# Optimization experiments

Hardware: AMD Instinct MI355X
Metric: run time of the kernel (lower is better)

The kernel has to match this reference:

```python
import jax, jax.numpy as jnp
import numpy as np
import math

D_MODEL = 1024
NUM_HEADS = 16
D_K = D_MODEL // NUM_HEADS
B, S = 2, 2048


def setup_inputs() -> dict:
    key = jax.random.key(0)
    ks = jax.random.split(key, 11)
    scale = 1.0 / math.sqrt(D_MODEL)
    inp = {
        "query": jax.random.normal(ks[0], (B, S, D_MODEL), jnp.float32),
        "key": jax.random.normal(ks[1], (B, S, D_MODEL), jnp.float32),
        "value": jax.random.normal(ks[2], (B, S, D_MODEL), jnp.float32),
        "Wq": jax.random.normal(ks[3], (D_MODEL, D_MODEL), jnp.float32) * scale,
        "bq": jnp.zeros((D_MODEL,), jnp.float32),
        "Wk": jax.random.normal(ks[4], (D_MODEL, D_MODEL), jnp.float32) * scale,
        "bk": jnp.zeros((D_MODEL,), jnp.float32),
        "Wv": jax.random.normal(ks[5], (D_MODEL, D_MODEL), jnp.float32) * scale,
        "bv": jnp.zeros((D_MODEL,), jnp.float32),
        "Wo": jax.random.normal(ks[6], (D_MODEL, D_MODEL), jnp.float32) * scale,
        "bo": jnp.zeros((D_MODEL,), jnp.float32),
    }
    return inp


def reference(query, key, value, Wq, bq, Wk, bk, Wv, bv, Wo, bo):
    b, s, _ = query.shape
    # QKV projections (torch Linear: x @ W.T + b)
    Q = query @ Wq.T + bq
    K = key @ Wk.T + bk
    V = value @ Wv.T + bv
    # [b, h, s, d_k]
    Q = Q.reshape(b, s, NUM_HEADS, D_K).transpose(0, 2, 1, 3)
    K = K.reshape(b, s, NUM_HEADS, D_K).transpose(0, 2, 1, 3)
    V = V.reshape(b, s, NUM_HEADS, D_K).transpose(0, 2, 1, 3)
    score = jnp.einsum("bhqd,bhkd->bhqk", Q, K) / math.sqrt(D_K)
    attn = jax.nn.softmax(score, axis=-1)
    out = jnp.einsum("bhqk,bhkd->bhqd", attn, V)
    out = out.transpose(0, 2, 1, 3).reshape(b, s, D_MODEL)
    return out @ Wo.T + bo
```

## Files before the change

### kernel.cpp

```cpp
#include <hip/hip_runtime.h>

#define NHEADS 16
#define SEQ    2048
#define BATCH  2
#define DMODEL 1024
#define MTOT   4096

typedef __attribute__((ext_vector_type(8)))  short short8;
typedef __attribute__((ext_vector_type(4)))  float f32x4;
typedef __attribute__((ext_vector_type(16))) float f32x16;

__device__ __forceinline__ unsigned short f32_to_bf16_rn(float x) {
  unsigned int u = __float_as_uint(x);
  u += 0x7fffu + ((u >> 16) & 1u);
  return (unsigned short)(u >> 16);
}

__device__ __forceinline__ unsigned cvt_pk_bf16(float lo, float hi_) {
  unsigned r;
  asm("v_cvt_pk_bf16_f32 %0, %1, %2" : "=v"(r) : "v"(lo), "v"(hi_));
  return r;
}

__device__ __forceinline__ void permlane32_swap(unsigned &a, unsigned &b) {
  asm("v_permlane32_swap_b32 %0, %1" : "+v"(a), "+v"(b));
}

__device__ __forceinline__ void async16(void* lds, const void* g) {
  __builtin_amdgcn_global_load_lds((const __attribute__((address_space(1))) unsigned int*)g,
                                   (__attribute__((address_space(3))) unsigned int*)lds, 16, 0, 0);
}

__global__ void cvt_bf16_kernel(const float* __restrict__ x0, const float* __restrict__ x1,
                                const float* __restrict__ x2,
                                const float* __restrict__ w0, const float* __restrict__ w1,
                                const float* __restrict__ w2, const float* __restrict__ w3,
                                unsigned short* __restrict__ obase)
{
  const int e = (blockIdx.x*256 + threadIdx.x)*8;
  const float* src;
  int local;
  if (e < 3*4194304) {
    const int t = e >> 22;
    src = t==0 ? x0 : t==1 ? x1 : x2;
    local = e & (4194304-1);
    src += local;
    local += t << 22;
  } else {
    const int f = e - 3*4194304;
    const int t = f >> 20;
    src = t==0 ? w0 : t==1 ? w1 : t==2 ? w2 : w3;
    src += (f & (1048576-1));
    local = e;
  }
  const float4 v0 = *(const float4*)(src);
  const float4 v1 = *(const float4*)(src + 4);
  union { unsigned short u[8]; uint4 v; } r;
  r.u[0] = f32_to_bf16_rn(v0.x); r.u[1] = f32_to_bf16_rn(v0.y);
  r.u[2] = f32_to_bf16_rn(v0.z); r.u[3] = f32_to_bf16_rn(v0.w);
  r.u[4] = f32_to_bf16_rn(v1.x); r.u[5] = f32_to_bf16_rn(v1.y);
  r.u[6] = f32_to_bf16_rn(v1.z); r.u[7] = f32_to_bf16_rn(v1.w);
  *(uint4*)(obase + local) = r.v;
}

template<int BM>
__device__ __forceinline__ void gemm_core(const unsigned short* __restrict__ A,
                                          const unsigned short* __restrict__ W,
                                          unsigned short* sA, unsigned short* sB,
                                          int m0, int n0, f32x4 (&acc)[BM/32][4])
{
  constexpr int MI = BM/32;
  const int t = threadIdx.x;
  const int lane = t & 63;
  const int wv = t >> 6;
  const int wm = wv >> 1, wn = wv & 1;
  const int lr = lane & 15, lk = lane >> 4;

  for (int kt = 0; kt < DMODEL/64; ++kt) {
    #pragma unroll
    for (int g = 0; g < MI; ++g) {
      const int o  = g*4096 + t*16;
      const int so = o ^ (((o >> 7) & 7) << 4);
      const int row = so >> 7, colE = (so & 127) >> 1;
      async16((char*)sA + o, A + (size_t)(m0 + row)*DMODEL + kt*64 + colE);
    }
    #pragma unroll
    for (int g = 0; g < 4; ++g) {
      const int o  = g*4096 + t*16;
      const int so = o ^ (((o >> 7) & 7) << 4);
      const int row = so >> 7, colE = (so & 127) >> 1;
      async16((char*)sB + o, W + (size_t)(n0 + row)*DMODEL + kt*64 + colE);
    }
    __syncthreads();
    #pragma unroll
    for (int ks = 0; ks < 2; ++ks) {
      short8 af[MI], bf[4];
      #pragma unroll
      for (int mi = 0; mi < MI; ++mi) {
        const int row = wm*(BM/2) + mi*16 + lr;
        const int sl  = (ks*4 + lk) ^ (row & 7);
        af[mi] = *(const short8*)(sA + row*64 + sl*8);
      }
      #pragma unroll
      for (int ni = 0; ni < 4; ++ni) {
        const int row = wn*64 + ni*16 + lr;
        const int sl  = (ks*4 + lk) ^ (row & 7);
        bf[ni] = *(const short8*)(sB + row*64 + sl*8);
      }
      #pragma unroll
      for (int mi = 0; mi < MI; ++mi)
        #pragma unroll
        for (int ni = 0; ni < 4; ++ni)
          acc[mi][ni] = __builtin_amdgcn_mfma_f32_16x16x32_bf16(af[mi], bf[ni], acc[mi][ni], 0, 0, 0);
    }
    __syncthreads();
  }
}

__global__ __launch_bounds__(256, 2)
void qkv_gemm_kernel(const unsigned short* __restrict__ Xq, const unsigned short* __restrict__ Xk,
                     const unsigned short* __restrict__ Xv,
                     const unsigned short* __restrict__ Wq, const unsigned short* __restrict__ Wk,
                     const unsigned short* __restrict__ Wv,
                     const float* __restrict__ bq, const float* __restrict__ bk,
                     const float* __restrict__ bv,
                     unsigned short* __restrict__ Qp, unsigned short* __restrict__ Kp,
                     unsigned short* __restrict__ Vtp)
{
  constexpr int BM = 128;
  constexpr int MI = BM/32;
  __shared__ __align__(16) unsigned short sA[BM*64];
  __shared__ __align__(16) unsigned short sB[128*64];

  const int m0   = blockIdx.x * BM;
  const int nabs = blockIdx.y * 128;
  const int wsel = nabs >> 10;
  const int n0   = nabs & 1023;
  const unsigned short* A = wsel==0 ? Xq : wsel==1 ? Xk : Xv;
  const unsigned short* W = wsel==0 ? Wq : wsel==1 ? Wk : Wv;
  const float* bias       = wsel==0 ? bq : wsel==1 ? bk : bv;
  unsigned short* dst     = wsel==0 ? Qp : wsel==1 ? Kp : Vtp;

  f32x4 acc[MI][4];
  #pragma unroll
  for (int mi = 0; mi < MI; ++mi)
    #pragma unroll
    for (int ni = 0; ni < 4; ++ni)
      acc[mi][ni] = {0.f, 0.f, 0.f, 0.f};

  gemm_core<BM>(A, W, sA, sB, m0, n0, acc);

  const int t = threadIdx.x, lane = t & 63, wvx = t >> 6;
  const int wm = wvx >> 1, wn = wvx & 1;
  const int lr = lane & 15, lk = lane >> 4;
  const float qscale = (wsel == 0) ? 0.125f * 1.4426950408889634f : 1.0f;

  #pragma unroll
  for (int ni = 0; ni < 4; ++ni) {
    const int nn = n0 + wn*64 + ni*16 + lr;
    const float badd = bias[nn];
    const int hh = nn >> 6, d = nn & 63;
    #pragma unroll
    for (int mi = 0; mi < MI; ++mi) {
      #pragma unroll
      for (int r = 0; r < 4; ++r) {
        const int m = m0 + wm*(BM/2) + mi*16 + lk*4 + r;
        const int bb = m >> 11, s = m & 2047;
        const float v = (acc[mi][ni][r] + badd) * qscale;
        size_t idx;
        if (wsel == 2) idx = (((size_t)bb*NHEADS + hh)*64 + d)*SEQ + s;
        else           idx = (((size_t)bb*NHEADS + hh)*SEQ + s)*64 + d;
        dst[idx] = f32_to_bf16_rn(v);
      }
    }
  }
}

__global__ __launch_bounds__(256, 2)
void attn_kernel(const unsigned short* __restrict__ Qp, const unsigned short* __restrict__ Kp,
                 const unsigned short* __restrict__ Vtp, unsigned short* __restrict__ Op)
{
  __shared__ __align__(16) unsigned short sm[16384];

  const int t = threadIdx.x, lane = t & 63, w = t >> 6;
  const int lq = lane & 31, hi = lane >> 5;
  const int qt = blockIdx.x, h = blockIdx.y, b = blockIdx.z;
  const size_t bh = (size_t)b*NHEADS + h;
  const unsigned short* Qh = Qp  + bh*SEQ*64;
  const unsigned short* Kh = Kp  + bh*SEQ*64;
  const unsigned short* Vh = Vtp + bh*64*SEQ;
  const int q0 = qt*128 + w*32;

  short8 qf[4];
  #pragma unroll
  for (int ks = 0; ks < 4; ++ks)
    qf[ks] = *(const short8*)(Qh + (size_t)(q0 + lq)*64 + ks*16 + hi*8);

  union { unsigned u[4]; short8 s; } ones;
  #pragma unroll
  for (int i = 0; i < 4; ++i) ones.u[i] = 0x3F803F80u;

  const unsigned short* srcp;
  size_t sstride;
  if (w < 2) { srcp = Kh + (size_t)(w*32 + lq)*64 + hi*8;        sstride = 64*64; }
  else       { srcp = Vh + (size_t)((w-2)*32 + lq)*2048 + hi*8;  sstride = 64;    }

  #pragma unroll
  for (int i = 0; i < 4; ++i)
    async16((char*)sm + w*4096 + i*1024, srcp + i*16);
  srcp += sstride;
  asm volatile("s_waitcnt vmcnt(0)" ::: "memory");
  __syncthreads();

  f32x16 o[2], ls;
  #pragma unroll
  for (int d = 0; d < 2; ++d)
    #pragma unroll
    for (int r = 0; r < 16; ++r) o[d][r] = 0.f;
  #pragma unroll
  for (int r = 0; r < 16; ++r) ls[r] = 0.f;

  #pragma unroll 2
  for (int kt = 0; kt < SEQ/64; ++kt) {
    if (kt + 1 < SEQ/64) {
      const int nb = ((kt + 1) & 1) * 16384;
      #pragma unroll
      for (int i = 0; i < 4; ++i)
        async16((char*)sm + nb + w*4096 + i*1024, srcp + i*16);
      srcp += sstride;
    }
    const unsigned short* base  = sm + (kt & 1)*8192;
    const unsigned short* vbase = base + 4096;

    f32x16 st[2];
    #pragma unroll
    for (int s = 0; s < 2; ++s)
      #pragma unroll
      for (int r = 0; r < 16; ++r) st[s][r] = 0.f;
    __builtin_amdgcn_s_setprio(1);
    #pragma unroll
    for (int sub = 0; sub < 2; ++sub)
      #pragma unroll
      for (int ks = 0; ks < 4; ++ks) {
        const short8 kf = *(const short8*)(base + (sub*4 + ks)*512 + lane*8);
        st[sub] = __builtin_amdgcn_mfma_f32_32x32x16_bf16(kf, qf[ks], st[sub], 0, 0, 0);
      }
    __builtin_amdgcn_s_setprio(0);

    #pragma unroll
    for (int s = 0; s < 2; ++s)
      #pragma unroll
      for (int r = 0; r < 16; ++r)
        st[s][r] = __builtin_amdgcn_exp2f(st[s][r]);

    #pragma unroll
    for (int sub = 0; sub < 2; ++sub) {
      union { unsigned u[4]; short8 s; } pA, pB;
      {
        unsigned x0 = cvt_pk_bf16(st[sub][0],  st[sub][1]);
        unsigned x1 = cvt_pk_bf16(st[sub][2],  st[sub][3]);
        unsigned y0 = cvt_pk_bf16(st[sub][4],  st[sub][5]);
        unsigned y1 = cvt_pk_bf16(st[sub][6],  st[sub][7]);
        permlane32_swap(x0, y0);
        permlane32_swap(x1, y1);
        pA.u[0] = x0; pA.u[1] = x1; pA.u[2] = y0; pA.u[3] = y1;
        unsigned z0 = cvt_pk_bf16(st[sub][8],  st[sub][9]);
        unsigned z1 = cvt_pk_bf16(st[sub][10], st[sub][11]);
        unsigned w0 = cvt_pk_bf16(st[sub][12], st[sub][13]);
        unsigned w1 = cvt_pk_bf16(st[sub][14], st[sub][15]);
        permlane32_swap(z0, w0);
        permlane32_swap(z1, w1);
        pB.u[0] = z0; pB.u[1] = z1; pB.u[2] = w0; pB.u[3] = w1;
      }
      const short8 v00 = *(const short8*)(vbase + (0*4 + 2*sub    )*512 + lane*8);
      const short8 v01 = *(const short8*)(vbase + (0*4 + 2*sub + 1)*512 + lane*8);
      const short8 v10 = *(const short8*)(vbase + (1*4 + 2*sub    )*512 + lane*8);
      const short8 v11 = *(const short8*)(vbase + (1*4 + 2*sub + 1)*512 + lane*8);
      __builtin_amdgcn_s_setprio(1);
      o[0] = __builtin_amdgcn_mfma_f32_32x32x16_bf16(v00, pA.s, o[0], 0, 0, 0);
      o[1] = __builtin_amdgcn_mfma_f32_32x32x16_bf16(v10, pA.s, o[1], 0, 0, 0);
      ls   = __builtin_amdgcn_mfma_f32_32x32x16_bf16(ones.s, pA.s, ls, 0, 0, 0);
      o[0] = __builtin_amdgcn_mfma_f32_32x32x16_bf16(v01, pB.s, o[0], 0, 0, 0);
      o[1] = __builtin_amdgcn_mfma_f32_32x32x16_bf16(v11, pB.s, o[1], 0, 0, 0);
      ls   = __builtin_amdgcn_mfma_f32_32x32x16_bf16(ones.s, pB.s, ls, 0, 0, 0);
      __builtin_amdgcn_s_setprio(0);
    }
    asm volatile("s_waitcnt vmcnt(0)" ::: "memory");
    __syncthreads();
  }

  const float inv = __builtin_amdgcn_rcpf(ls[0]);
  unsigned short* orow = Op + ((size_t)b*SEQ + q0 + lq)*DMODEL + h*64;
  #pragma unroll
  for (int dblk = 0; dblk < 2; ++dblk)
    #pragma unroll
    for (int g = 0; g < 4; ++g) {
      union { unsigned short us[4]; uint2 v; } pk;
      #pragma unroll
      for (int r = 0; r < 4; ++r) pk.us[r] = f32_to_bf16_rn(o[dblk][g*4 + r] * inv);
      *(uint2*)(orow + dblk*32 + g*8 + hi*4) = pk.v;
    }
}

__global__ __launch_bounds__(256, 2)
void oproj_gemm_kernel(const unsigned short* __restrict__ Oin, const unsigned short* __restrict__ Wo,
                       const float* __restrict__ bo, float* __restrict__ out)
{
  constexpr int BM = 64;
  constexpr int MI = BM/32;
  __shared__ __align__(16) unsigned short sA[BM*64];
  __shared__ __align__(16) unsigned short sB[128*64];
  const int m0 = blockIdx.x * BM;
  const int n0 = blockIdx.y * 128;

  f32x4 acc[MI][4];
  #pragma unroll
  for (int mi = 0; mi < MI; ++mi)
    #pragma unroll
    for (int ni = 0; ni < 4; ++ni)
      acc[mi][ni] = {0.f,0.f,0.f,0.f};

  gemm_core<BM>(Oin, Wo, sA, sB, m0, n0, acc);

  const int t = threadIdx.x, lane = t & 63, wvx = t >> 6;
  const int wm = wvx >> 1, wn = wvx & 1;
  const int lr = lane & 15, lk = lane >> 4;

  #pragma unroll
  for (int ni = 0; ni < 4; ++ni) {
    const int nn = n0 + wn*64 + ni*16 + lr;
    const float badd = bo[nn];
    #pragma unroll
    for (int mi = 0; mi < MI; ++mi)
      #pragma unroll
      for (int r = 0; r < 4; ++r) {
        const int m = m0 + wm*(BM/2) + mi*16 + lk*4 + r;
        out[(size_t)m*DMODEL + nn] = acc[mi][ni][r] + badd;
      }
  }
}

extern "C" void kernel_launch(void* const* d_in, const int* in_sizes, int n_in,
                              void* d_out, int out_size, void* d_ws, size_t ws_size,
                              hipStream_t stream) {
  const float* query = (const float*)d_in[0];
  const float* key   = (const float*)d_in[1];
  const float* value = (const float*)d_in[2];
  const float* Wq    = (const float*)d_in[3];
  const float* bq    = (const float*)d_in[4];
  const float* Wk    = (const float*)d_in[5];
  const float* bk    = (const float*)d_in[6];
  const float* Wv    = (const float*)d_in[7];
  const float* bv    = (const float*)d_in[8];
  const float* Wo    = (const float*)d_in[9];
  const float* bo    = (const float*)d_in[10];

  const size_t NX = (size_t)MTOT*DMODEL;
  const size_t NW = (size_t)DMODEL*DMODEL;
  unsigned short* w   = (unsigned short*)d_ws;
  unsigned short* Xq  = w;
  unsigned short* Xk  = Xq  + NX;
  unsigned short* Xv  = Xk  + NX;
  unsigned short* Wqp = Xv  + NX;
  unsigned short* Wkp = Wqp + NW;
  unsigned short* Wvp = Wkp + NW;
  unsigned short* Wop = Wvp + NW;
  unsigned short* Qp  = Wop + NW;
  unsigned short* Kp  = Qp  + NX;
  unsigned short* Vtp = Kp  + NX;
  unsigned short* Opb = Vtp + NX;

  cvt_bf16_kernel<<<dim3(8192), 256, 0, stream>>>(
      query, key, value, Wq, Wk, Wv, Wo, w);
  qkv_gemm_kernel<<<dim3(32, 24), 256, 0, stream>>>(
      Xq, Xk, Xv, Wqp, Wkp, Wvp, bq, bk, bv, Qp, Kp, Vtp);
  attn_kernel<<<dim3(16, 16, 2), 256, 0, stream>>>(Qp, Kp, Vtp, Opb);
  oproj_gemm_kernel<<<dim3(64, 8), 256, 0, stream>>>(Opb, Wop, bo, (float*)d_out);
}
```

Baseline: 118.0 us.

## Split attention over key halves, add combine kernel, coalesce V-transpose stores

The attention kernel now splits each query tile's key range into two halves, launching 1024 blocks with an XCD-aware block remap, and writes unnormalised partial outputs and row sums that a new combine kernel merges and normalises. Row sums are accumulated with VALU adds instead of extra ones-vector MFMAs. The QKV GEMM stages its V output through shared memory so the transposed V writes are coalesced 16-byte stores, and occupancy hints are raised. The split adds an extra kernel launch and more intermediate traffic in exchange for better CU utilisation and fewer MFMAs.

```diff
diff --git a/kernel.cpp b/kernel.cpp
--- a/kernel.cpp
+++ b/kernel.cpp
@@ -117,7 +117,7 @@
   }
 }
 
-__global__ __launch_bounds__(256, 2)
+__global__ __launch_bounds__(256, 3)
 void qkv_gemm_kernel(const unsigned short* __restrict__ Xq, const unsigned short* __restrict__ Xk,
                      const unsigned short* __restrict__ Xv,
                      const unsigned short* __restrict__ Wq, const unsigned short* __restrict__ Wk,
@@ -129,8 +129,9 @@
 {
   constexpr int BM = 128;
   constexpr int MI = BM/32;
-  __shared__ __align__(16) unsigned short sA[BM*64];
-  __shared__ __align__(16) unsigned short sB[128*64];
+  __shared__ __align__(16) unsigned short smem[17024];
+  unsigned short* sA = smem;
+  unsigned short* sB = smem + 8192;
 
   const int m0   = blockIdx.x * BM;
   const int nabs = blockIdx.y * 128;
@@ -139,7 +140,6 @@
   const unsigned short* A = wsel==0 ? Xq : wsel==1 ? Xk : Xv;
   const unsigned short* W = wsel==0 ? Wq : wsel==1 ? Wk : Wv;
   const float* bias       = wsel==0 ? bq : wsel==1 ? bk : bv;
-  unsigned short* dst     = wsel==0 ? Qp : wsel==1 ? Kp : Vtp;
 
   f32x4 acc[MI][4];
   #pragma unroll
@@ -153,41 +153,68 @@
   const int t = threadIdx.x, lane = t & 63, wvx = t >> 6;
   const int wm = wvx >> 1, wn = wvx & 1;
   const int lr = lane & 15, lk = lane >> 4;
-  const float qscale = (wsel == 0) ? 0.125f * 1.4426950408889634f : 1.0f;
-
-  #pragma unroll
-  for (int ni = 0; ni < 4; ++ni) {
-    const int nn = n0 + wn*64 + ni*16 + lr;
-    const float badd = bias[nn];
-    const int hh = nn >> 6, d = nn & 63;
-    #pragma unroll
-    for (int mi = 0; mi < MI; ++mi) {
-      #pragma unroll
-      for (int r = 0; r < 4; ++r) {
-        const int m = m0 + wm*(BM/2) + mi*16 + lk*4 + r;
-        const int bb = m >> 11, s = m & 2047;
-        const float v = (acc[mi][ni][r] + badd) * qscale;
-        size_t idx;
-        if (wsel == 2) idx = (((size_t)bb*NHEADS + hh)*64 + d)*SEQ + s;
-        else           idx = (((size_t)bb*NHEADS + hh)*SEQ + s)*64 + d;
-        dst[idx] = f32_to_bf16_rn(v);
-      }
-    }
-  }
-}
-
-__global__ __launch_bounds__(256, 2)
+
+  if (wsel == 2) {
+    #pragma unroll
+    for (int ni = 0; ni < 4; ++ni) {
+      const float badd = bias[n0 + wn*64 + ni*16 + lr];
+      #pragma unroll
+      for (int mi = 0; mi < MI; ++mi)
+        #pragma unroll
+        for (int r = 0; r < 4; ++r) {
+          const int ml = wm*(BM/2) + mi*16 + lk*4 + r;
+          smem[(wn*64 + ni*16 + lr)*132 + ml] = f32_to_bf16_rn(acc[mi][ni][r] + badd);
+        }
+    }
+    __syncthreads();
+    const int bb = m0 >> 11, s0 = m0 & 2047;
+    const int jr = (t & 15)*8, nr = t >> 4;
+    #pragma unroll
+    for (int pass = 0; pass < 8; ++pass) {
+      const int n  = pass*16 + nr;
+      const int nn = n0 + n, hh = nn >> 6, d = nn & 63;
+      const short8 v = *(const short8*)(smem + n*132 + jr);
+      *(short8*)(Vtp + (((size_t)bb*NHEADS + hh)*64 + d)*SEQ + s0 + jr) = v;
+    }
+  } else {
+    unsigned short* dst = wsel==0 ? Qp : Kp;
+    const float qscale = (wsel == 0) ? 0.125f * 1.4426950408889634f : 1.0f;
+    #pragma unroll
+    for (int ni = 0; ni < 4; ++ni) {
+      const int nn = n0 + wn*64 + ni*16 + lr;
+      const float badd = bias[nn];
+      const int hh = nn >> 6, d = nn & 63;
+      #pragma unroll
+      for (int mi = 0; mi < MI; ++mi) {
+        #pragma unroll
+        for (int r = 0; r < 4; ++r) {
+          const int m = m0 + wm*(BM/2) + mi*16 + lk*4 + r;
+          const int bb = m >> 11, s = m & 2047;
+          const float v = (acc[mi][ni][r] + badd) * qscale;
+          dst[(((size_t)bb*NHEADS + hh)*SEQ + s)*64 + d] = f32_to_bf16_rn(v);
+        }
+      }
+    }
+  }
+}
+
+__global__ __launch_bounds__(256, 4)
 void attn_kernel(const unsigned short* __restrict__ Qp, const unsigned short* __restrict__ Kp,
-                 const unsigned short* __restrict__ Vtp, unsigned short* __restrict__ Op)
+                 const unsigned short* __restrict__ Vtp,
+                 unsigned short* __restrict__ Opar, float* __restrict__ Lpar)
 {
   __shared__ __align__(16) unsigned short sm[16384];
+  constexpr int NT = 1024/64;
 
   const int t = threadIdx.x, lane = t & 63, w = t >> 6;
   const int lq = lane & 31, hi = lane >> 5;
-  const int qt = blockIdx.x, h = blockIdx.y, b = blockIdx.z;
+  const int f   = blockIdx.x;
+  const int wid = (f & 7)*128 + (f >> 3);
+  const int qt = wid & 15, h = (wid >> 4) & 15, b = (wid >> 8) & 1, half = wid >> 9;
+
   const size_t bh = (size_t)b*NHEADS + h;
   const unsigned short* Qh = Qp  + bh*SEQ*64;
-  const unsigned short* Kh = Kp  + bh*SEQ*64;
+  const unsigned short* Kh = Kp  + bh*SEQ*64 + (size_t)half*1024*64;
   const unsigned short* Vh = Vtp + bh*64*SEQ;
   const int q0 = qt*128 + w*32;
 
@@ -196,14 +223,10 @@
   for (int ks = 0; ks < 4; ++ks)
     qf[ks] = *(const short8*)(Qh + (size_t)(q0 + lq)*64 + ks*16 + hi*8);
 
-  union { unsigned u[4]; short8 s; } ones;
-  #pragma unroll
-  for (int i = 0; i < 4; ++i) ones.u[i] = 0x3F803F80u;
-
   const unsigned short* srcp;
   size_t sstride;
-  if (w < 2) { srcp = Kh + (size_t)(w*32 + lq)*64 + hi*8;        sstride = 64*64; }
-  else       { srcp = Vh + (size_t)((w-2)*32 + lq)*2048 + hi*8;  sstride = 64;    }
+  if (w < 2) { srcp = Kh + (size_t)(w*32 + lq)*64 + hi*8;                      sstride = 64*64; }
+  else       { srcp = Vh + (size_t)((w-2)*32 + lq)*2048 + half*1024 + hi*8;    sstride = 64;    }
 
   #pragma unroll
   for (int i = 0; i < 4; ++i)
@@ -212,17 +235,16 @@
   asm volatile("s_waitcnt vmcnt(0)" ::: "memory");
   __syncthreads();
 
-  f32x16 o[2], ls;
+  f32x16 o[2];
+  float lsa[4] = {0.f, 0.f, 0.f, 0.f};
   #pragma unroll
   for (int d = 0; d < 2; ++d)
     #pragma unroll
     for (int r = 0; r < 16; ++r) o[d][r] = 0.f;
-  #pragma unroll
-  for (int r = 0; r < 16; ++r) ls[r] = 0.f;
 
   #pragma unroll 2
-  for (int kt = 0; kt < SEQ/64; ++kt) {
-    if (kt + 1 < SEQ/64) {
+  for (int kt = 0; kt < NT; ++kt) {
+    if (kt + 1 < NT) {
       const int nb = ((kt + 1) & 1) * 16384;
       #pragma unroll
       for (int i = 0; i < 4; ++i)
@@ -250,8 +272,11 @@
     #pragma unroll
     for (int s = 0; s < 2; ++s)
       #pragma unroll
-      for (int r = 0; r < 16; ++r)
-        st[s][r] = __builtin_amdgcn_exp2f(st[s][r]);
+      for (int r = 0; r < 16; ++r) {
+        const float p = __builtin_amdgcn_exp2f(st[s][r]);
+        st[s][r] = p;
+        lsa[r & 3] += p;
+      }
 
     #pragma unroll
     for (int sub = 0; sub < 2; ++sub) {
@@ -279,27 +304,58 @@
       __builtin_amdgcn_s_setprio(1);
       o[0] = __builtin_amdgcn_mfma_f32_32x32x16_bf16(v00, pA.s, o[0], 0, 0, 0);
       o[1] = __builtin_amdgcn_mfma_f32_32x32x16_bf16(v10, pA.s, o[1], 0, 0, 0);
-      ls   = __builtin_amdgcn_mfma_f32_32x32x16_bf16(ones.s, pA.s, ls, 0, 0, 0);
       o[0] = __builtin_amdgcn_mfma_f32_32x32x16_bf16(v01, pB.s, o[0], 0, 0, 0);
       o[1] = __builtin_amdgcn_mfma_f32_32x32x16_bf16(v11, pB.s, o[1], 0, 0, 0);
-      ls   = __builtin_amdgcn_mfma_f32_32x32x16_bf16(ones.s, pB.s, ls, 0, 0, 0);
       __builtin_amdgcn_s_setprio(0);
     }
     asm volatile("s_waitcnt vmcnt(0)" ::: "memory");
     __syncthreads();
   }
 
-  const float inv = __builtin_amdgcn_rcpf(ls[0]);
-  unsigned short* orow = Op + ((size_t)b*SEQ + q0 + lq)*DMODEL + h*64;
+  float lsum = (lsa[0] + lsa[1]) + (lsa[2] + lsa[3]);
+  lsum += __shfl_xor(lsum, 32);
+  if (lane < 32)
+    Lpar[half*65536 + b*32768 + h*2048 + q0 + lq] = lsum;
+
+  const size_t row = (size_t)b*SEQ + q0 + lq;
+  unsigned short* orow = Opar + ((size_t)half*MTOT + row)*DMODEL + h*64;
   #pragma unroll
   for (int dblk = 0; dblk < 2; ++dblk)
     #pragma unroll
     for (int g = 0; g < 4; ++g) {
       union { unsigned short us[4]; uint2 v; } pk;
       #pragma unroll
-      for (int r = 0; r < 4; ++r) pk.us[r] = f32_to_bf16_rn(o[dblk][g*4 + r] * inv);
+      for (int r = 0; r < 4; ++r) pk.us[r] = f32_to_bf16_rn(o[dblk][g*4 + r]);
       *(uint2*)(orow + dblk*32 + g*8 + hi*4) = pk.v;
     }
+}
+
+__global__ void combine_kernel(const unsigned short* __restrict__ Opar,
+                               const float* __restrict__ Lpar,
+                               unsigned short* __restrict__ Op)
+{
+  const int flat = blockIdx.x*256 + threadIdx.x;
+  const int row  = flat >> 8;
+  const int col4 = flat & 255;
+  const int b = row >> 11, q = row & 2047, h = col4 >> 4;
+
+  const uint2 a = *(const uint2*)(Opar + (size_t)row*DMODEL + col4*4);
+  const uint2 c = *(const uint2*)(Opar + (size_t)(MTOT + row)*DMODEL + col4*4);
+  const float l0 = Lpar[b*32768 + h*2048 + q];
+  const float l1 = Lpar[65536 + b*32768 + h*2048 + q];
+  const float inv = __builtin_amdgcn_rcpf(l0 + l1);
+
+  union { unsigned u[2]; uint2 v; } ua, uc, r;
+  ua.v = a; uc.v = c;
+  union { unsigned short us[4]; uint2 v; } out;
+  #pragma unroll
+  for (int j = 0; j < 4; ++j) {
+    const unsigned va = ((j & 1) ? (ua.u[j >> 1] >> 16) : (ua.u[j >> 1] & 0xffffu)) << 16;
+    const unsigned vc = ((j & 1) ? (uc.u[j >> 1] >> 16) : (uc.u[j >> 1] & 0xffffu)) << 16;
+    const float s = (__uint_as_float(va) + __uint_as_float(vc)) * inv;
+    out.us[j] = f32_to_bf16_rn(s);
+  }
+  *(uint2*)(Op + (size_t)row*DMODEL + col4*4) = out.v;
 }
 
 __global__ __launch_bounds__(256, 2)
@@ -369,11 +425,14 @@
   unsigned short* Kp  = Qp  + NX;
   unsigned short* Vtp = Kp  + NX;
   unsigned short* Opb = Vtp + NX;
+  unsigned short* Opar = w;
+  float*          Lpar = (float*)(w + 2*NX);
 
   cvt_bf16_kernel<<<dim3(8192), 256, 0, stream>>>(
       query, key, value, Wq, Wk, Wv, Wo, w);
   qkv_gemm_kernel<<<dim3(32, 24), 256, 0, stream>>>(
       Xq, Xk, Xv, Wqp, Wkp, Wvp, bq, bk, bv, Qp, Kp, Vtp);
-  attn_kernel<<<dim3(16, 16, 2), 256, 0, stream>>>(Qp, Kp, Vtp, Opb);
+  attn_kernel<<<dim3(1024), 256, 0, stream>>>(Qp, Kp, Vtp, Opar, Lpar);
+  combine_kernel<<<dim3(4096), 256, 0, stream>>>(Opar, Lpar, Opb);
   oproj_gemm_kernel<<<dim3(64, 8), 256, 0, stream>>>(Opb, Wop, bo, (float*)d_out);
 }
```

Result: slower. 120.5 us (+2.1%).
